# Performance work log

Hardware: AMD Instinct MI355X
Metric: run time of the kernel (lower is better)

The kernel has to match this reference:

```python
import jax, jax.numpy as jnp
import numpy as np

N = 100000
E = 1600000
D = 128


def setup_inputs() -> dict:
    key = jax.random.key(0)
    k1, k2, k3, k4, k5, k6, k7 = jax.random.split(key, 7)
    adj_row = jax.random.randint(k1, (E,), 0, N, dtype=jnp.int64 if jax.config.jax_enable_x64 else jnp.int32)
    adj_col = jax.random.randint(k2, (E,), 0, N, dtype=jnp.int64 if jax.config.jax_enable_x64 else jnp.int32)
    adj_val = jax.random.uniform(k3, (E,), dtype=jnp.float32)
    embeds = jax.random.normal(k4, (N, D), dtype=jnp.float32)
    s = 1.0 / np.sqrt(D)  # ~xavier scale for square matrices
    qTrans = jax.random.normal(k5, (D, D), dtype=jnp.float32) * s
    kTrans = jax.random.normal(k6, (D, D), dtype=jnp.float32) * s
    vTrans = jax.random.normal(k7, (D, D), dtype=jnp.float32) * s
    return {"adj_row": adj_row, "adj_col": adj_col, "adj_val": adj_val,
            "embeds": embeds, "qTrans": qTrans, "kTrans": kTrans, "vTrans": vTrans}


def reference(adj_row, adj_col, adj_val, embeds, qTrans, kTrans, vTrans):
    n = embeds.shape[0]
    latdim = qTrans.shape[1]
    # projections, reshaped to [N, H, latdim]; H = 1 since W is latdim x latdim
    qE = (embeds @ qTrans).reshape(n, -1, latdim)
    kE = (embeds @ kTrans).reshape(n, -1, latdim)
    vE = (embeds @ vTrans).reshape(n, -1, latdim)
    att = jnp.einsum('bhd,bhd->bh', qE, kE)
    att = jnp.clip(att, -10.0, 10.0)
    expAtt = jnp.exp(att)
    attNorm = expAtt / (expAtt.sum(axis=-1, keepdims=True) + 1e-8)
    resEmbeds = jnp.einsum('bh,bhd->bd', attNorm, vE).reshape(-1, latdim)
    # sparse spmm: out[i] = sum_{e: row[e]==i} val[e] * resEmbeds[col[e]]
    msgs = adj_val[:, None] * resEmbeds[adj_col]  # [E, latdim]
    out = jax.ops.segment_sum(msgs, adj_row, num_segments=n)
    return out, attNorm
```

## Files before the change

### kernel.cpp

```cpp
#include <hip/hip_runtime.h>

#define D 128
#define BROWS 128
#define BCAP 2432
#define CHUNK 4096
#define NBMAX 800
#define ELL 48

typedef __bf16 bf16x8 __attribute__((ext_vector_type(8)));
typedef float f32x4 __attribute__((ext_vector_type(4)));

union BF8 { ushort u[8]; uint4 q; bf16x8 v; };

__device__ __forceinline__ ushort f2bf(float f) {
    uint u = __float_as_uint(f);
    uint r = (u + 0x7FFFu + ((u >> 16) & 1u)) >> 16;
    return (ushort)r;
}

__global__ __launch_bounds__(256) void wprep_kernel(
    const float* __restrict__ vW,
    uint4* __restrict__ wfrag)
{
    int t = blockIdx.x * 256 + threadIdx.x;
    int g = t >> 6, l = t & 63;
    if (g >= 32) return;
    int kt = g >> 3, ct = g & 7;
    int krow = kt * 32 + (l >> 4) * 8;
    int col  = ct * 16 + (l & 15);
    BF8 b;
    #pragma unroll
    for (int j = 0; j < 8; ++j) b.u[j] = f2bf(vW[(krow + j) * D + col]);
    wfrag[g * 64 + l] = b.q;
}

__global__ __launch_bounds__(256) void proj_v_mfma(
    const float* __restrict__ embeds,
    const uint4* __restrict__ wfrag,
    ushort* __restrict__ resb,
    float*  __restrict__ attnorm,
    int n)
{
    __shared__ uint4 wlds[32 * 64];

    const int t = threadIdx.x;
    const int w = t >> 6;
    const int l = t & 63;
    const int lr = l & 15;
    const int lk = l >> 4;

    #pragma unroll
    for (int i = 0; i < 8; ++i) wlds[i * 256 + t] = wfrag[i * 256 + t];
    __syncthreads();

    const bf16x8* wb = (const bf16x8*)wlds;
    const int ntiles = (n + 15) >> 4;

    for (int tile = blockIdx.x * 4 + w; tile < ntiles; tile += gridDim.x * 4) {
        int r0 = tile * 16;
        int arow = r0 + lr; if (arow >= n) arow = n - 1;

        bf16x8 a[4];
        #pragma unroll
        for (int kt = 0; kt < 4; ++kt) {
            const float4* src = (const float4*)(embeds + (size_t)arow * D + kt * 32 + lk * 8);
            float4 f0 = src[0];
            float4 f1 = src[1];
            BF8 cvt;
            cvt.u[0] = f2bf(f0.x); cvt.u[1] = f2bf(f0.y);
            cvt.u[2] = f2bf(f0.z); cvt.u[3] = f2bf(f0.w);
            cvt.u[4] = f2bf(f1.x); cvt.u[5] = f2bf(f1.y);
            cvt.u[6] = f2bf(f1.z); cvt.u[7] = f2bf(f1.w);
            a[kt] = cvt.v;
        }

        f32x4 acc[8];
        #pragma unroll
        for (int ct = 0; ct < 8; ++ct) acc[ct] = (f32x4){0.f, 0.f, 0.f, 0.f};

        #pragma unroll
        for (int ct = 0; ct < 8; ++ct)
            #pragma unroll
            for (int kt = 0; kt < 4; ++kt)
                acc[ct] = __builtin_amdgcn_mfma_f32_16x16x32_bf16(
                    a[kt], wb[(kt * 8 + ct) * 64 + l], acc[ct], 0, 0, 0);

        #pragma unroll
        for (int r = 0; r < 4; ++r) {
            int row = r0 + 4 * lk + r;
            if (row < n) {
                if (lr == 0) attnorm[row] = 1.0f;
                #pragma unroll
                for (int ct = 0; ct < 8; ++ct)
                    resb[(size_t)row * D + ct * 16 + lr] = f2bf(acc[ct][r]);
            }
        }
    }
}

__global__ __launch_bounds__(256) void bin_kernel(
    const int*   __restrict__ rowp,
    const int*   __restrict__ colp,
    const float* __restrict__ valp,
    int*   __restrict__ gcursor,
    uint2* __restrict__ recs,
    int ne, int nbuck)
{
    __shared__ uint  cnt[NBMAX];
    __shared__ uint  lbase[NBMAX];
    __shared__ uint  gpos[NBMAX];
    __shared__ uint  rk[NBMAX];
    __shared__ uint  wsum[4];
    __shared__ uint2 stage[CHUNK];

    const int tid  = threadIdx.x;
    const int w    = tid >> 6;
    const int lane = tid & 63;
    const int base = blockIdx.x * CHUNK;
    const int nrec = min(CHUNK, ne - base);

    for (int i = tid; i < nbuck; i += 256) { cnt[i] = 0; rk[i] = 0; }
    __syncthreads();

    for (int i = tid; i < nrec; i += 256) {
        int b = rowp[base + i] >> 7;
        atomicAdd(&cnt[b], 1u);
    }
    __syncthreads();

    int s0 = tid * 4;
    uint c0 = (s0 + 0 < nbuck) ? cnt[s0 + 0] : 0u;
    uint c1 = (s0 + 1 < nbuck) ? cnt[s0 + 1] : 0u;
    uint c2 = (s0 + 2 < nbuck) ? cnt[s0 + 2] : 0u;
    uint c3 = (s0 + 3 < nbuck) ? cnt[s0 + 3] : 0u;
    uint partial = c0 + c1 + c2 + c3;
    uint p = partial;
    #pragma unroll
    for (int s = 1; s < 64; s <<= 1) {
        uint x = __shfl_up(p, s, 64);
        if (lane >= s) p += x;
    }
    if (lane == 63) wsum[w] = p;
    __syncthreads();
    uint woff = 0;
    for (int i = 0; i < w; ++i) woff += wsum[i];
    uint excl = woff + p - partial;
    if (s0 + 0 < nbuck) lbase[s0 + 0] = excl;
    if (s0 + 1 < nbuck) lbase[s0 + 1] = excl + c0;
    if (s0 + 2 < nbuck) lbase[s0 + 2] = excl + c0 + c1;
    if (s0 + 3 < nbuck) lbase[s0 + 3] = excl + c0 + c1 + c2;

    for (int b = tid; b < nbuck; b += 256)
        if (cnt[b]) gpos[b] = (uint)atomicAdd(&gcursor[b], (int)cnt[b]);
    __syncthreads();

    for (int i = tid; i < nrec; i += 256) {
        int e = base + i;
        int r = rowp[e];
        int b = r >> 7;
        uint w0  = ((uint)(r & 127) << 17) | (uint)colp[e];
        uint pos = lbase[b] + atomicAdd(&rk[b], 1u);
        stage[pos] = make_uint2(w0, __float_as_uint(valp[e]));
    }
    __syncthreads();

    for (int b = tid; b < nbuck; b += 256) {
        uint c = cnt[b];
        if (!c) continue;
        uint gp = gpos[b], lp = lbase[b];
        uint lim = (gp >= BCAP) ? 0u : min(c, (uint)BCAP - gp);
        uint2* dst = recs + (size_t)b * BCAP + gp;
        for (uint i = 0; i < lim; ++i) dst[i] = stage[lp + i];
    }
}

__global__ __launch_bounds__(512) void ellify_kernel(
    const uint2* __restrict__ recs,
    const int*   __restrict__ gcursor,
    uint2* __restrict__ ell,
    int*   __restrict__ deg,
    int n, int nbuck)
{
    __shared__ uint2 stage[BROWS * ELL];
    __shared__ uint  rcnt[BROWS];

    const int b   = blockIdx.x;
    const int tid = threadIdx.x;

    {
        uint4* s4 = (uint4*)stage;
        for (int i = tid; i < BROWS * ELL / 2; i += 512) s4[i] = make_uint4(0u, 0u, 0u, 0u);
        if (tid < BROWS) rcnt[tid] = 0u;
    }
    __syncthreads();

    const int cnt = min(gcursor[b], BCAP);
    const uint2* rb = recs + (size_t)b * BCAP;
    for (int i = tid; i < cnt; i += 512) {
        uint2 rec = rb[i];
        int rl = (int)(rec.x >> 17);
        uint pos = atomicAdd(&rcnt[rl], 1u);
        if (pos < ELL) stage[rl * ELL + pos] = make_uint2(rec.x & 0x1FFFFu, rec.y);
    }
    __syncthreads();

    const int row0 = b * BROWS;
    const int rows_here = min(BROWS, n - row0);
    for (int rr = tid >> 3; rr < rows_here; rr += 64) {
        int cnt8 = ((int)min(rcnt[rr], (uint)ELL) + 7) & ~7;
        uint2* drow = ell + (size_t)(row0 + rr) * ELL;
        for (int j = tid & 7; j < cnt8; j += 8) drow[j] = stage[rr * ELL + j];
    }
    for (int i = tid; i < rows_here; i += 512) deg[row0 + i] = (int)min(rcnt[i], (uint)ELL);
}

__global__ __launch_bounds__(256) void gather_ell(
    const uint2* __restrict__ ell, const int* __restrict__ deg,
    const ushort* __restrict__ resb, float* __restrict__ out, int n)
{
    int wid  = (blockIdx.x * 256 + threadIdx.x) >> 6;
    int lane = threadIdx.x & 63;
    if (wid >= n) return;

    int cnt  = deg[wid];
    int cnt8 = (cnt + 7) & ~7;

    uint2 c = make_uint2(0u, 0u);
    if (lane < cnt8) c = ell[(size_t)wid * ELL + lane];

    const uint* resv = (const uint*)resb;
    float2 acc = make_float2(0.f, 0.f);

    for (int k0 = 0; k0 < cnt8; k0 += 8) {
        #pragma unroll
        for (int k = 0; k < 8; ++k) {
            uint  cc = (uint)__shfl((int)c.x, k0 + k, 64);
            float vv = __int_as_float(__shfl((int)c.y, k0 + k, 64));
            uint  m  = resv[(size_t)cc * 64 + lane];
            acc.x = fmaf(vv, __uint_as_float(m << 16), acc.x);
            acc.y = fmaf(vv, __uint_as_float(m & 0xFFFF0000u), acc.y);
        }
    }
    ((float2*)out)[(size_t)wid * 64 + lane] = acc;
}

extern "C" void kernel_launch(void* const* d_in, const int* in_sizes, int n_in,
                              void* d_out, int out_size, void* d_ws, size_t ws_size,
                              hipStream_t stream)
{
    const int*   adj_row = (const int*)d_in[0];
    const int*   adj_col = (const int*)d_in[1];
    const float* adj_val = (const float*)d_in[2];
    const float* embeds  = (const float*)d_in[3];
    const float* vW      = (const float*)d_in[6];

    const int E_ = in_sizes[0];
    const int N_ = in_sizes[3] / D;
    const int nbuck = (N_ + BROWS - 1) / BROWS;

    float* out     = (float*)d_out;
    float* attnorm = out + (size_t)N_ * D;

    uint2* recs = (uint2*)d_out;

    char*   ws      = (char*)d_ws;
    ushort* resb    = (ushort*)ws;
    uint2*  ell     = (uint2*)(ws + (size_t)N_ * D * 2);
    int*    deg     = (int*)((char*)ell + (size_t)N_ * ELL * 8);
    int*    gcursor = deg + N_;
    uint4*  wfrag   = (uint4*)(gcursor + nbuck);

    hipMemsetAsync(gcursor, 0, (size_t)nbuck * sizeof(int), stream);

    wprep_kernel<<<8, 256, 0, stream>>>(vW, wfrag);

    int nblk_bin = (E_ + CHUNK - 1) / CHUNK;
    bin_kernel<<<nblk_bin, 256, 0, stream>>>(adj_row, adj_col, adj_val,
                                             gcursor, recs, E_, nbuck);

    ellify_kernel<<<nbuck, 512, 0, stream>>>(recs, gcursor, ell, deg, N_, nbuck);

    proj_v_mfma<<<1024, 256, 0, stream>>>(embeds, wfrag, resb, attnorm, N_);

    int nblocks_gather = ((size_t)N_ * 64 + 255) / 256;
    gather_ell<<<nblocks_gather, 256, 0, stream>>>(ell, deg, resb, out, N_);
}
```

Measured before the change: 129.4 us.

## Merge weight prep into binning and projection into ELL build kernel

Folds the weight-fragment prep kernel into the binning kernel as extra blocks, and merges the ELL build with the V projection GEMM into one launch whose block ranges do different work. The aim is fewer kernel launches and letting the independent projection overlap the memory-bound ELL build. The cost is a shared-memory union sized by the larger role, and the projection now uses 512-thread blocks with 8 waves per block and a different grid size.

```diff
diff --git a/kernel.cpp b/kernel.cpp
--- a/kernel.cpp
+++ b/kernel.cpp
@@ -6,6 +6,7 @@
 #define CHUNK 4096
 #define NBMAX 800
 #define ELL 48
+#define PROJ_BLOCKS 512
 
 typedef __bf16 bf16x8 __attribute__((ext_vector_type(8)));
 typedef float f32x4 __attribute__((ext_vector_type(4)));
@@ -18,94 +19,32 @@
     return (ushort)r;
 }
 
-__global__ __launch_bounds__(256) void wprep_kernel(
-    const float* __restrict__ vW,
-    uint4* __restrict__ wfrag)
-{
-    int t = blockIdx.x * 256 + threadIdx.x;
-    int g = t >> 6, l = t & 63;
-    if (g >= 32) return;
-    int kt = g >> 3, ct = g & 7;
-    int krow = kt * 32 + (l >> 4) * 8;
-    int col  = ct * 16 + (l & 15);
-    BF8 b;
-    #pragma unroll
-    for (int j = 0; j < 8; ++j) b.u[j] = f2bf(vW[(krow + j) * D + col]);
-    wfrag[g * 64 + l] = b.q;
-}
-
-__global__ __launch_bounds__(256) void proj_v_mfma(
-    const float* __restrict__ embeds,
-    const uint4* __restrict__ wfrag,
-    ushort* __restrict__ resb,
-    float*  __restrict__ attnorm,
-    int n)
-{
-    __shared__ uint4 wlds[32 * 64];
-
-    const int t = threadIdx.x;
-    const int w = t >> 6;
-    const int l = t & 63;
-    const int lr = l & 15;
-    const int lk = l >> 4;
-
-    #pragma unroll
-    for (int i = 0; i < 8; ++i) wlds[i * 256 + t] = wfrag[i * 256 + t];
-    __syncthreads();
-
-    const bf16x8* wb = (const bf16x8*)wlds;
-    const int ntiles = (n + 15) >> 4;
-
-    for (int tile = blockIdx.x * 4 + w; tile < ntiles; tile += gridDim.x * 4) {
-        int r0 = tile * 16;
-        int arow = r0 + lr; if (arow >= n) arow = n - 1;
-
-        bf16x8 a[4];
-        #pragma unroll
-        for (int kt = 0; kt < 4; ++kt) {
-            const float4* src = (const float4*)(embeds + (size_t)arow * D + kt * 32 + lk * 8);
-            float4 f0 = src[0];
-            float4 f1 = src[1];
-            BF8 cvt;
-            cvt.u[0] = f2bf(f0.x); cvt.u[1] = f2bf(f0.y);
-            cvt.u[2] = f2bf(f0.z); cvt.u[3] = f2bf(f0.w);
-            cvt.u[4] = f2bf(f1.x); cvt.u[5] = f2bf(f1.y);
-            cvt.u[6] = f2bf(f1.z); cvt.u[7] = f2bf(f1.w);
-            a[kt] = cvt.v;
-        }
-
-        f32x4 acc[8];
-        #pragma unroll
-        for (int ct = 0; ct < 8; ++ct) acc[ct] = (f32x4){0.f, 0.f, 0.f, 0.f};
-
-        #pragma unroll
-        for (int ct = 0; ct < 8; ++ct)
-            #pragma unroll
-            for (int kt = 0; kt < 4; ++kt)
-                acc[ct] = __builtin_amdgcn_mfma_f32_16x16x32_bf16(
-                    a[kt], wb[(kt * 8 + ct) * 64 + l], acc[ct], 0, 0, 0);
-
-        #pragma unroll
-        for (int r = 0; r < 4; ++r) {
-            int row = r0 + 4 * lk + r;
-            if (row < n) {
-                if (lr == 0) attnorm[row] = 1.0f;
-                #pragma unroll
-                for (int ct = 0; ct < 8; ++ct)
-                    resb[(size_t)row * D + ct * 16 + lr] = f2bf(acc[ct][r]);
-            }
-        }
-    }
-}
-
-__global__ __launch_bounds__(256) void bin_kernel(
+__global__ __launch_bounds__(256) void bin_wprep_kernel(
     const int*   __restrict__ rowp,
     const int*   __restrict__ colp,
     const float* __restrict__ valp,
+    const float* __restrict__ vW,
     int*   __restrict__ gcursor,
     uint2* __restrict__ recs,
-    int ne, int nbuck)
-{
+    uint4* __restrict__ wfrag,
+    int ne, int nbuck, int nblk_bin)
+{
+    const int tid = threadIdx.x;
+
+    if ((int)blockIdx.x >= nblk_bin) {
+        int t = (blockIdx.x - nblk_bin) * 256 + tid;
+        int g = t >> 6, l = t & 63;
+        if (g >= 32) return;
+        int kt = g >> 3, ct = g & 7;
+        int krow = kt * 32 + (l >> 4) * 8;
+        int col  = ct * 16 + (l & 15);
+        BF8 b;
+        #pragma unroll
+        for (int j = 0; j < 8; ++j) b.u[j] = f2bf(vW[(krow + j) * D + col]);
+        wfrag[g * 64 + l] = b.q;
+        return;
+    }
+
     __shared__ uint  cnt[NBMAX];
     __shared__ uint  lbase[NBMAX];
     __shared__ uint  gpos[NBMAX];
@@ -113,7 +52,6 @@
     __shared__ uint  wsum[4];
     __shared__ uint2 stage[CHUNK];
 
-    const int tid  = threadIdx.x;
     const int w    = tid >> 6;
     const int lane = tid & 63;
     const int base = blockIdx.x * CHUNK;
@@ -174,44 +112,108 @@
     }
 }
 
-__global__ __launch_bounds__(512) void ellify_kernel(
-    const uint2* __restrict__ recs,
-    const int*   __restrict__ gcursor,
+union SharedU {
+    struct { uint2 stage[BROWS * ELL]; uint rcnt[BROWS]; } e;
+    uint4 wlds[32 * 64];
+};
+
+__global__ __launch_bounds__(512) void ellify_proj_kernel(
+    const uint2*  __restrict__ recs,
+    const int*    __restrict__ gcursor,
+    const float*  __restrict__ embeds,
+    const uint4*  __restrict__ wfrag,
     uint2* __restrict__ ell,
     int*   __restrict__ deg,
+    ushort* __restrict__ resb,
+    float*  __restrict__ attnorm,
     int n, int nbuck)
 {
-    __shared__ uint2 stage[BROWS * ELL];
-    __shared__ uint  rcnt[BROWS];
-
-    const int b   = blockIdx.x;
+    __shared__ SharedU sh;
     const int tid = threadIdx.x;
 
-    {
-        uint4* s4 = (uint4*)stage;
-        for (int i = tid; i < BROWS * ELL / 2; i += 512) s4[i] = make_uint4(0u, 0u, 0u, 0u);
-        if (tid < BROWS) rcnt[tid] = 0u;
-    }
-    __syncthreads();
-
-    const int cnt = min(gcursor[b], BCAP);
-    const uint2* rb = recs + (size_t)b * BCAP;
-    for (int i = tid; i < cnt; i += 512) {
-        uint2 rec = rb[i];
-        int rl = (int)(rec.x >> 17);
-        uint pos = atomicAdd(&rcnt[rl], 1u);
-        if (pos < ELL) stage[rl * ELL + pos] = make_uint2(rec.x & 0x1FFFFu, rec.y);
-    }
-    __syncthreads();
-
-    const int row0 = b * BROWS;
-    const int rows_here = min(BROWS, n - row0);
-    for (int rr = tid >> 3; rr < rows_here; rr += 64) {
-        int cnt8 = ((int)min(rcnt[rr], (uint)ELL) + 7) & ~7;
-        uint2* drow = ell + (size_t)(row0 + rr) * ELL;
-        for (int j = tid & 7; j < cnt8; j += 8) drow[j] = stage[rr * ELL + j];
-    }
-    for (int i = tid; i < rows_here; i += 512) deg[row0 + i] = (int)min(rcnt[i], (uint)ELL);
+    if ((int)blockIdx.x < nbuck) {
+        const int b = blockIdx.x;
+        {
+            uint4* s4 = (uint4*)sh.e.stage;
+            for (int i = tid; i < BROWS * ELL / 2; i += 512) s4[i] = make_uint4(0u, 0u, 0u, 0u);
+            if (tid < BROWS) sh.e.rcnt[tid] = 0u;
+        }
+        __syncthreads();
+
+        const int cnt = min(gcursor[b], BCAP);
+        const uint2* rb = recs + (size_t)b * BCAP;
+        for (int i = tid; i < cnt; i += 512) {
+            uint2 rec = rb[i];
+            int rl = (int)(rec.x >> 17);
+            uint pos = atomicAdd(&sh.e.rcnt[rl], 1u);
+            if (pos < ELL) sh.e.stage[rl * ELL + pos] = make_uint2(rec.x & 0x1FFFFu, rec.y);
+        }
+        __syncthreads();
+
+        const int row0 = b * BROWS;
+        const int rows_here = min(BROWS, n - row0);
+        for (int rr = tid >> 3; rr < rows_here; rr += 64) {
+            int cnt8 = ((int)min(sh.e.rcnt[rr], (uint)ELL) + 7) & ~7;
+            uint2* drow = ell + (size_t)(row0 + rr) * ELL;
+            for (int j = tid & 7; j < cnt8; j += 8) drow[j] = sh.e.stage[rr * ELL + j];
+        }
+        for (int i = tid; i < rows_here; i += 512) deg[row0 + i] = (int)min(sh.e.rcnt[i], (uint)ELL);
+        return;
+    }
+
+    const int pb = blockIdx.x - nbuck;
+    const int w  = tid >> 6;
+    const int l  = tid & 63;
+    const int lr = l & 15;
+    const int lk = l >> 4;
+
+    #pragma unroll
+    for (int i = 0; i < 4; ++i) sh.wlds[i * 512 + tid] = wfrag[i * 512 + tid];
+    __syncthreads();
+
+    const bf16x8* wb = (const bf16x8*)sh.wlds;
+    const int ntiles = (n + 15) >> 4;
+
+    for (int tile = pb * 8 + w; tile < ntiles; tile += PROJ_BLOCKS * 8) {
+        int r0 = tile * 16;
+        int arow = r0 + lr; if (arow >= n) arow = n - 1;
+
+        bf16x8 a[4];
+        #pragma unroll
+        for (int kt = 0; kt < 4; ++kt) {
+            const float4* src = (const float4*)(embeds + (size_t)arow * D + kt * 32 + lk * 8);
+            float4 f0 = src[0];
+            float4 f1 = src[1];
+            BF8 cvt;
+            cvt.u[0] = f2bf(f0.x); cvt.u[1] = f2bf(f0.y);
+            cvt.u[2] = f2bf(f0.z); cvt.u[3] = f2bf(f0.w);
+            cvt.u[4] = f2bf(f1.x); cvt.u[5] = f2bf(f1.y);
+            cvt.u[6] = f2bf(f1.z); cvt.u[7] = f2bf(f1.w);
+            a[kt] = cvt.v;
+        }
+
+        f32x4 acc[8];
+        #pragma unroll
+        for (int ct = 0; ct < 8; ++ct) acc[ct] = (f32x4){0.f, 0.f, 0.f, 0.f};
+
+        #pragma unroll
+        for (int ct = 0; ct < 8; ++ct)
+            #pragma unroll
+            for (int kt = 0; kt < 4; ++kt)
+                acc[ct] = __builtin_amdgcn_mfma_f32_16x16x32_bf16(
+                    a[kt], wb[(kt * 8 + ct) * 64 + l], acc[ct], 0, 0, 0);
+
+        #pragma unroll
+        for (int r = 0; r < 4; ++r) {
+            int row = r0 + 4 * lk + r;
+            if (row < n) {
+                if (lr == 0) attnorm[row] = 1.0f;
+                #pragma unroll
+                for (int ct = 0; ct < 8; ++ct)
+                    resb[(size_t)row * D + ct * 16 + lr] = f2bf(acc[ct][r]);
+            }
+        }
+    }
 }
 
 __global__ __launch_bounds__(256) void gather_ell(
@@ -272,15 +274,12 @@
 
     hipMemsetAsync(gcursor, 0, (size_t)nbuck * sizeof(int), stream);
 
-    wprep_kernel<<<8, 256, 0, stream>>>(vW, wfrag);
-
     int nblk_bin = (E_ + CHUNK - 1) / CHUNK;
-    bin_kernel<<<nblk_bin, 256, 0, stream>>>(adj_row, adj_col, adj_val,
-                                             gcursor, recs, E_, nbuck);
-
-    ellify_kernel<<<nbuck, 512, 0, stream>>>(recs, gcursor, ell, deg, N_, nbuck);
-
-    proj_v_mfma<<<1024, 256, 0, stream>>>(embeds, wfrag, resb, attnorm, N_);
+    bin_wprep_kernel<<<nblk_bin + 8, 256, 0, stream>>>(
+        adj_row, adj_col, adj_val, vW, gcursor, recs, wfrag, E_, nbuck, nblk_bin);
+
+    ellify_proj_kernel<<<nbuck + PROJ_BLOCKS, 512, 0, stream>>>(
+        recs, gcursor, embeds, wfrag, ell, deg, resb, attnorm, N_, nbuck);
 
     int nblocks_gather = ((size_t)N_ * 64 + 255) / 256;
     gather_ell<<<nblocks_gather, 256, 0, stream>>>(ell, deg, resb, out, N_);
```

New measurement: 130.3 us. About the same (+0.7%).
